# Performance work log

Measured on AMD Instinct MI355X. Metric: run time of the kernel, lower is better.

## Reference

```python
import jax, jax.numpy as jnp
import numpy as np

B, T, C = 2, 2048, 1024
H = 16
D = C // H  # head_dim = 64
EPS = 1e-06
MAX_SEQ = 2048


def make_rotary(dim, max_seq_len, base=10000):
    inv_freq = 1.0 / (base ** (jnp.arange(0, dim, 2, dtype=jnp.float32) / dim))
    pos = jnp.arange(max_seq_len, dtype=jnp.float32)
    sinusoid = jnp.einsum('i,j->ij', pos, inv_freq)  # (S, dim//2)
    return jnp.sin(sinusoid), jnp.cos(sinusoid)


def apply_rotary(x, sin, cos):
    # x: (B, T, H, D); sin/cos: (MAX_SEQ, D//2)
    t = x.shape[1]
    s = sin[:t][:, None, :]  # (T,1,D//2) broadcasts over B and H
    c = cos[:t][:, None, :]
    d = x.shape[-1]
    x1, x2 = x[..., :d // 2], x[..., d // 2:]
    return jnp.concatenate([x1 * c - x2 * s, x2 * c + x1 * s], axis=-1)


def yat_dense(x, kernel, bias, alpha, eps=EPS):
    # Yat layer: squared dot product over squared euclidean distance.
    dot = x @ kernel                                   # (..., out)
    x_sq = jnp.sum(x * x, axis=-1, keepdims=True)      # (..., 1)
    k_sq = jnp.sum(kernel * kernel, axis=0)            # (out,)
    dist = x_sq + k_sq - 2.0 * dot
    y = (dot * dot) / (dist + eps)
    out_f = kernel.shape[1]
    scale = (jnp.sqrt(jnp.float32(out_f)) / jnp.log(1.0 + jnp.float32(out_f))) ** alpha
    return y * scale + bias


def setup_inputs() -> dict:
    key = jax.random.key(0)
    ks = jax.random.split(key, 7)
    x = jax.random.normal(ks[0], (B, T, C), dtype=jnp.float32)
    mask = jnp.tril(jnp.ones((T, T), dtype=bool))[None].repeat(B, axis=0)  # (B,T,T) causal
    s = 1.0 / np.sqrt(C)
    w_attn = jax.random.normal(ks[1], (C, 3 * C), dtype=jnp.float32) * s
    b_attn = jnp.zeros((3 * C,), dtype=jnp.float32)
    a_attn = jnp.ones((1,), dtype=jnp.float32)
    w_proj = jax.random.normal(ks[2], (C, C), dtype=jnp.float32) * s
    b_proj = jnp.zeros((C,), dtype=jnp.float32)
    a_proj = jnp.ones((1,), dtype=jnp.float32)
    return {"x": x, "mask": mask, "w_attn": w_attn, "b_attn": b_attn,
            "a_attn": a_attn, "w_proj": w_proj, "b_proj": b_proj, "a_proj": a_proj}


def reference(x, mask, w_attn, b_attn, a_attn, w_proj, b_proj, a_proj):
    b, t, c = x.shape
    sin, cos = make_rotary(D, MAX_SEQ)
    qkv = yat_dense(x, w_attn, b_attn, a_attn)          # (B,T,3C)
    qkv = qkv.reshape(b, t, 3, H, D)
    q, k, v = jnp.moveaxis(qkv, 2, 0)                   # each (B,T,H,D)
    q = apply_rotary(q, sin, cos)
    k = apply_rotary(k, sin, cos)
    # heads-major layout for attention
    q = q.transpose(0, 2, 1, 3)                          # (B,H,T,D)
    k = k.transpose(0, 2, 1, 3)
    v = v.transpose(0, 2, 1, 3)
    scale = jnp.sqrt(jnp.float32(D))
    attn = jnp.einsum('bhqd,bhkd->bhqk', q, k) / scale   # (B,H,T,T)
    m = mask[:, None, :, :]                              # (B,1,T,T)
    attn = jnp.where(m, attn, jnp.finfo(jnp.float32).min)
    attn = jax.nn.softmax(attn, axis=-1)
    # dropout is identity in deterministic/eval mode
    out = jnp.einsum('bhqk,bhkd->bhqd', attn, v)         # (B,H,T,D)
    out = out.transpose(0, 2, 1, 3).reshape(b, t, c)     # (B,T,C)
    out = yat_dense(out, w_proj, b_proj, a_proj)
    return out
```

## Files before the change

kernel.cpp:

```cpp
#include <hip/hip_runtime.h>
#include <math.h>

#define TSEQ  2048
#define BATCH 2
#define NH    16
#define HD    64
#define CDIM  1024
#define N3C   3072
#define EPSY  1e-6f

typedef unsigned short u16;
typedef unsigned int u32;
typedef __attribute__((ext_vector_type(8))) short bf16x8;
typedef __attribute__((ext_vector_type(4))) float f32x4;

#define MFMA16(a, b, c) __builtin_amdgcn_mfma_f32_16x16x32_bf16(a, b, c, 0, 0, 0)

__device__ __forceinline__ u16 f2bf(float f) {
    unsigned u = __float_as_uint(f);
    return (u16)((u + 0x7fffu + ((u >> 16) & 1u)) >> 16);
}
__device__ __forceinline__ float bf2f(u16 h) {
    return __uint_as_float(((unsigned)h) << 16);
}
__device__ __forceinline__ void gload16(const void* g, void* l) {
    __builtin_amdgcn_global_load_lds(
        (const __attribute__((address_space(1))) unsigned int*)g,
        (__attribute__((address_space(3))) unsigned int*)l, 16, 0, 0);
}

__global__ __launch_bounds__(256) void prep_kernel(
    const float* __restrict__ x, const float* __restrict__ wa,
    const float* __restrict__ wp, u16* __restrict__ Ahi,
    u16* __restrict__ Wthi, u16* __restrict__ Wphi,
    float* __restrict__ ksq, float* __restrict__ xsq,
    float* __restrict__ osq, float2* __restrict__ ropeSC) {
    __shared__ float smem[64 * 68];
    int bid = blockIdx.x, tid = threadIdx.x;

    if (bid < 4096) {
        int lane = tid & 63, wv = tid >> 6;
        size_t base = (size_t)bid * CDIM + tid * 4;
        float4 v = *(const float4*)(x + base);
        ushort4 hi;
        hi.x = f2bf(v.x); hi.y = f2bf(v.y); hi.z = f2bf(v.z); hi.w = f2bf(v.w);
        *(ushort4*)(Ahi + base) = hi;
        float s = v.x * v.x + v.y * v.y + v.z * v.z + v.w * v.w;
        #pragma unroll
        for (int off = 32; off; off >>= 1) s += __shfl_down(s, off, 64);
        if (lane == 0) smem[wv] = s;
        __syncthreads();
        if (tid == 0) xsq[bid] = smem[0] + smem[1] + smem[2] + smem[3];
    } else if (bid < 5120) {
        const float* W; u16* Whi; int K, N, bx, by;
        if (bid < 4864) {
            int t = bid - 4096; W = wa; Whi = Wthi; K = CDIM; N = N3C;
            bx = t % 48; by = t / 48;
        } else {
            int t = bid - 4864; W = wp; Whi = Wphi; K = CDIM; N = CDIM;
            bx = t % 16; by = t / 16;
        }
        int k0 = by * 64, n0 = bx * 64;
        int r = tid >> 4, c4 = (tid & 15) * 4;
        #pragma unroll
        for (int i = 0; i < 4; ++i) {
            int k = k0 + r + i * 16;
            float4 v = *(const float4*)(W + (size_t)k * N + n0 + c4);
            *(float4*)&smem[(r + i * 16) * 68 + c4] = v;
        }
        __syncthreads();
        int n = tid >> 4, k4 = (tid & 15) * 4;
        #pragma unroll
        for (int i = 0; i < 4; ++i) {
            int nn = n + i * 16;
            ushort4 hi;
            hi.x = f2bf(smem[(k4 + 0) * 68 + nn]);
            hi.y = f2bf(smem[(k4 + 1) * 68 + nn]);
            hi.z = f2bf(smem[(k4 + 2) * 68 + nn]);
            hi.w = f2bf(smem[(k4 + 3) * 68 + nn]);
            *(ushort4*)(Whi + (size_t)(n0 + nn) * K + k0 + k4) = hi;
        }
    } else if (bid < 5184) {
        int b2 = bid - 5120;
        int c = tid & 63, kq = tid >> 6;
        const float* W; int N, col, outoff;
        if (b2 < 48) { W = wa; N = N3C;  col = b2 * 64 + c;        outoff = 0;   }
        else         { W = wp; N = CDIM; col = (b2 - 48) * 64 + c; outoff = N3C; }
        float s = 0.f;
        int i0 = kq * 256;
        #pragma unroll 4
        for (int i = i0; i < i0 + 256; ++i) {
            float v = W[(size_t)i * N + col];
            s = fmaf(v, v, s);
        }
        smem[tid] = s;
        __syncthreads();
        if (kq == 0)
            ksq[outoff + col] = smem[c] + smem[64 + c] + smem[128 + c] + smem[192 + c];
    } else {
        int idx = (bid - 5184) * 256 + tid;
        if (idx < BATCH * TSEQ) osq[idx] = 0.f;
        int t = idx >> 5, j = idx & 31;
        float inv = exp2f(-(float)j * 0.4152410118609203f);
        float ang = (float)t * inv;
        ropeSC[idx] = make_float2(cosf(ang), sinf(ang));
    }
}

__global__ __launch_bounds__(256, 4) void gemm1_fused(
    const u16* __restrict__ Ah, const u16* __restrict__ Bh,
    const float* __restrict__ bias, const float* __restrict__ rowsq,
    const float* __restrict__ colsq, const float* __restrict__ alphap,
    const float2* __restrict__ ropeSC,
    u16* __restrict__ Qb, u16* __restrict__ Kb, u16* __restrict__ Vt) {
    constexpr int BK = 32;
    const int K = CDIM;
    __shared__ u16 Ash[128 * BK], Bsh[128 * BK];
    int tid = threadIdx.x;
    int lane = tid & 63, wv = tid >> 6;
    int quad = lane >> 4, l15 = lane & 15;
    int wr = wv >> 1, wc = wv & 1;
    int bm = blockIdx.y * 128, bn = blockIdx.x * 128;
    int rsub = lane >> 2;
    int lc8 = (lane & 3) * 8;
    int gc8 = (((lane & 3) - (rsub >> 1)) & 3) * 8;
    int pf8 = ((quad + (l15 >> 1)) & 3) * 8;

    f32x4 acc[4][4];
    #pragma unroll
    for (int i = 0; i < 4; ++i)
        #pragma unroll
        for (int j = 0; j < 4; ++j) acc[i][j] = (f32x4){0.f, 0.f, 0.f, 0.f};

    for (int kt = 0; kt < K; kt += BK) {
        #pragma unroll
        for (int i = 0; i < 2; ++i) {
            int r = i * 64 + wv * 16 + rsub;
            gload16(Ah + (size_t)(bm + r) * K + kt + gc8, &Ash[r * BK + lc8]);
            gload16(Bh + (size_t)(bn + r) * K + kt + gc8, &Bsh[r * BK + lc8]);
        }
        __syncthreads();
        bf16x8 fah[4], fbh[4];
        #pragma unroll
        for (int i = 0; i < 4; ++i)
            fah[i] = *(const bf16x8*)&Ash[(wr * 64 + i * 16 + l15) * BK + pf8];
        #pragma unroll
        for (int j = 0; j < 4; ++j)
            fbh[j] = *(const bf16x8*)&Bsh[(wc * 64 + j * 16 + l15) * BK + pf8];
        #pragma unroll
        for (int i = 0; i < 4; ++i)
            #pragma unroll
            for (int j = 0; j < 4; ++j)
                acc[i][j] = MFMA16(fah[i], fbh[j], acc[i][j]);
        __syncthreads();
    }

    float alpha = alphap[0];
    float scale = powf(sqrtf((float)N3C) / logf(1.0f + (float)N3C), alpha);
    int segc0 = bn + wc * 64;
    int seg = segc0 >> 10;
    int h = (segc0 >> 6) & 15;
    int bglob = bm >> 11;
    int bh = bglob * NH + h;

    if (seg < 2) {
        u16* dst = (seg == 0) ? Qb : Kb;
        float qs = (seg == 0) ? 0.125f : 1.0f;
        #pragma unroll
        for (int i = 0; i < 4; ++i) {
            int tb = bm + wr * 64 + i * 16 + quad * 4;
            #pragma unroll
            for (int r = 0; r < 4; ++r) {
                int row = tb + r;
                int t = row & (TSEQ - 1);
                float rs = rowsq[row];
                float y[4];
                #pragma unroll
                for (int j = 0; j < 4; ++j) {
                    int col = segc0 + j * 16 + l15;
                    float dot = acc[i][j][r];
                    float dist = rs + colsq[col] - 2.0f * dot + EPSY;
                    y[j] = dot * dot / dist * scale + bias[col];
                }
                float2 sc0 = ropeSC[t * 32 + l15];
                float2 sc1 = ropeSC[t * 32 + 16 + l15];
                float c0 = sc0.x, s0 = sc0.y, c1 = sc1.x, s1 = sc1.y;
                size_t ob = ((size_t)bh * TSEQ + t) * HD;
                dst[ob + l15]      = f2bf((y[0] * c0 - y[2] * s0) * qs);
                dst[ob + 16 + l15] = f2bf((y[1] * c1 - y[3] * s1) * qs);
                dst[ob + 32 + l15] = f2bf((y[2] * c0 + y[0] * s0) * qs);
                dst[ob + 48 + l15] = f2bf((y[3] * c1 + y[1] * s1) * qs);
            }
        }
    } else {
        #pragma unroll
        for (int i = 0; i < 4; ++i) {
            int tb = bm + wr * 64 + i * 16 + quad * 4;
            int t0 = tb & (TSEQ - 1);
            #pragma unroll
            for (int j = 0; j < 4; ++j) {
                int col = segc0 + j * 16 + l15;
                int d = j * 16 + l15;
                float cs = colsq[col], bi = bias[col];
                ushort4 pk;
                u16* pp = (u16*)&pk;
                #pragma unroll
                for (int r = 0; r < 4; ++r) {
                    float dot = acc[i][j][r];
                    float dist = rowsq[tb + r] + cs - 2.0f * dot + EPSY;
                    pp[r] = f2bf(dot * dot / dist * scale + bi);
                }
                *(ushort4*)(Vt + ((size_t)bh * HD + d) * TSEQ + t0) = pk;
            }
        }
    }
}

__global__ __launch_bounds__(256, 4) void gemm_yat_mfma(
    const u16* __restrict__ Ah, const u16* __restrict__ Bh,
    const float* __restrict__ bias, const float* __restrict__ rowsq,
    const float* __restrict__ colsq, const float* __restrict__ alphap,
    float* __restrict__ outp, int M, int N, int K, float outf) {
    constexpr int BM = 128, BN = 64, BK = 32;
    __shared__ u16 Ash[BM * BK], Bsh[BN * BK];
    int tid = threadIdx.x;
    int lane = tid & 63, wv = tid >> 6;
    int quad = lane >> 4, l15 = lane & 15;
    int bm = blockIdx.y * BM, bn = blockIdx.x * BN;
    int rsub = lane >> 2;
    int lc8 = (lane & 3) * 8;
    int gc8 = (((lane & 3) - (rsub >> 1)) & 3) * 8;
    int pf8 = ((quad + (l15 >> 1)) & 3) * 8;

    f32x4 acc[2][4];
    #pragma unroll
    for (int i = 0; i < 2; ++i)
        #pragma unroll
        for (int j = 0; j < 4; ++j) acc[i][j] = (f32x4){0.f, 0.f, 0.f, 0.f};

    for (int kt = 0; kt < K; kt += BK) {
        #pragma unroll
        for (int i = 0; i < 2; ++i) {
            int r = i * 64 + wv * 16 + rsub;
            gload16(Ah + (size_t)(bm + r) * K + kt + gc8, &Ash[r * BK + lc8]);
        }
        {
            int r = wv * 16 + rsub;
            gload16(Bh + (size_t)(bn + r) * K + kt + gc8, &Bsh[r * BK + lc8]);
        }
        __syncthreads();
        bf16x8 fah[2], fbh[4];
        #pragma unroll
        for (int i = 0; i < 2; ++i)
            fah[i] = *(const bf16x8*)&Ash[(wv * 32 + i * 16 + l15) * BK + pf8];
        #pragma unroll
        for (int j = 0; j < 4; ++j)
            fbh[j] = *(const bf16x8*)&Bsh[(j * 16 + l15) * BK + pf8];
        #pragma unroll
        for (int i = 0; i < 2; ++i)
            #pragma unroll
            for (int j = 0; j < 4; ++j)
                acc[i][j] = MFMA16(fah[i], fbh[j], acc[i][j]);
        __syncthreads();
    }

    float alpha = alphap[0];
    float scale = powf(sqrtf(outf) / logf(1.0f + outf), alpha);
    #pragma unroll
    for (int j = 0; j < 4; ++j) {
        int col = bn + j * 16 + l15;
        float cs = colsq[col], bi = bias[col];
        #pragma unroll
        for (int i = 0; i < 2; ++i) {
            #pragma unroll
            for (int r = 0; r < 4; ++r) {
                int row = bm + wv * 32 + i * 16 + quad * 4 + r;
                float dot = acc[i][j][r];
                float dist = rowsq[row] + cs - 2.0f * dot + EPSY;
                outp[(size_t)row * N + col] = dot * dot / dist * scale + bi;
            }
        }
    }
}

__global__ __launch_bounds__(128) void attn_mfma(
    const u16* __restrict__ Qb, const u16* __restrict__ Kb,
    const u16* __restrict__ Vt, u16* __restrict__ Chi,
    float* __restrict__ osq) {
    __shared__ u16 Ksh[64 * 64];
    __shared__ u16 Vsh[64 * 64];
    int tid = threadIdx.x;
    int lane = tid & 63, wv = tid >> 6;
    int quad = lane >> 4, l15 = lane & 15;
    int bh = blockIdx.x;
    int b = bh >> 4, h = bh & 15;
    const u16* Qh = Qb + (size_t)bh * TSEQ * HD;
    const u16* Kh = Kb + (size_t)bh * TSEQ * HD;
    const u16* Vh = Vt + (size_t)bh * HD * TSEQ;
    const f32x4 zf = {0.f, 0.f, 0.f, 0.f};

    int qb = 31 - (blockIdx.y >> 1);
    int half = blockIdx.y & 1;
    int qw = qb * 64 + half * 32 + wv * 16;
    bf16x8 bq0 = *(const bf16x8*)(Qh + (size_t)(qw + l15) * HD + quad * 8);
    bf16x8 bq1 = *(const bf16x8*)(Qh + (size_t)(qw + l15) * HD + 32 + quad * 8);

    f32x4 o[4] = {zf, zf, zf, zf};
    float l = 0.f;

    for (int kt = 0; kt <= qb; ++kt) {
        int k0 = kt * 64;
        __syncthreads();
        #pragma unroll
        for (int p = 0; p < 4; ++p) {
            int lin = p * 128 + tid;
            int rowi = lin >> 3, ch = lin & 7;
            int gk = (ch + rowi) & 7;
            gload16(Kh + (size_t)(k0 + rowi) * HD + gk * 8, &Ksh[lin * 8]);
            gload16(Vh + (size_t)rowi * TSEQ + k0 + gk * 8, &Vsh[lin * 8]);
        }
        __syncthreads();

        f32x4 st[4];
        #pragma unroll
        for (int mt = 0; mt < 4; ++mt) {
            int key = mt * 16 + l15;
            bf16x8 a0 = *(const bf16x8*)&Ksh[key * 64 + ((quad - key) & 7) * 8];
            bf16x8 a1 = *(const bf16x8*)&Ksh[key * 64 + ((4 + quad - key) & 7) * 8];
            st[mt] = MFMA16(a0, bq0, zf);
            st[mt] = MFMA16(a1, bq1, st[mt]);
        }
        if (kt == qb) {
            int q = qw + l15;
            #pragma unroll
            for (int mt = 0; mt < 4; ++mt)
                #pragma unroll
                for (int r = 0; r < 4; ++r)
                    if (k0 + mt * 16 + quad * 4 + r > q) st[mt][r] = -1e30f;
        }
        u32 pp[4][2];
        #pragma unroll
        for (int mt = 0; mt < 4; ++mt) {
            float p0 = __expf(st[mt][0]);
            float p1 = __expf(st[mt][1]);
            float p2 = __expf(st[mt][2]);
            float p3 = __expf(st[mt][3]);
            l += (p0 + p1) + (p2 + p3);
            pp[mt][0] = (u32)f2bf(p0) | ((u32)f2bf(p1) << 16);
            pp[mt][1] = (u32)f2bf(p2) | ((u32)f2bf(p3) << 16);
        }
        #pragma unroll
        for (int s = 0; s < 2; ++s) {
            u32 bw[4];
            #pragma unroll
            for (int w = 0; w < 4; ++w) {
                int srcl = (((quad & 1) * 2 + (w >> 1)) << 4) + l15;
                u32 vlo = (u32)__shfl((int)pp[2 * s][w & 1], srcl, 64);
                u32 vhi = (u32)__shfl((int)pp[2 * s + 1][w & 1], srcl, 64);
                bw[w] = (quad & 2) ? vhi : vlo;
            }
            bf16x8 bfr;
            *(u32*)&((short*)&bfr)[0] = bw[0];
            *(u32*)&((short*)&bfr)[2] = bw[1];
            *(u32*)&((short*)&bfr)[4] = bw[2];
            *(u32*)&((short*)&bfr)[6] = bw[3];
            #pragma unroll
            for (int dt = 0; dt < 4; ++dt) {
                int d = dt * 16 + l15;
                bf16x8 av = *(const bf16x8*)&Vsh[d * 64 + ((s * 4 + quad - d) & 7) * 8];
                o[dt] = MFMA16(av, bfr, o[dt]);
            }
        }
    }

    l += __shfl_xor(l, 16, 64);
    l += __shfl_xor(l, 32, 64);
    float inv = 1.0f / l;
    int row = (b << 11) + qw + l15;
    float ss = 0.f;
    #pragma unroll
    for (int dt = 0; dt < 4; ++dt) {
        float v0 = o[dt][0] * inv, v1 = o[dt][1] * inv;
        float v2 = o[dt][2] * inv, v3 = o[dt][3] * inv;
        ss += v0 * v0 + v1 * v1 + v2 * v2 + v3 * v3;
        ushort4 pk;
        pk.x = f2bf(v0); pk.y = f2bf(v1); pk.z = f2bf(v2); pk.w = f2bf(v3);
        *(ushort4*)(Chi + (size_t)row * CDIM + h * HD + dt * 16 + quad * 4) = pk;
    }
    ss += __shfl_xor(ss, 16, 64);
    ss += __shfl_xor(ss, 32, 64);
    if (quad == 0) atomicAdd(osq + row, ss);
}

extern "C" void kernel_launch(void* const* d_in, const int* in_sizes, int n_in,
                              void* d_out, int out_size, void* d_ws, size_t ws_size,
                              hipStream_t stream) {
    const float* x      = (const float*)d_in[0];
    const float* w_attn = (const float*)d_in[2];
    const float* b_attn = (const float*)d_in[3];
    const float* a_attn = (const float*)d_in[4];
    const float* w_proj = (const float*)d_in[5];
    const float* b_proj = (const float*)d_in[6];
    const float* a_proj = (const float*)d_in[7];
    float* outp = (float*)d_out;

    char* ws = (char*)d_ws;
    float* ksq = (float*)(ws);
    float* xsq = (float*)(ws + 16384);
    float* osq = (float*)(ws + 32768);
    char* pA  = ws + 65536;
    u16* Ahi = (u16*)pA;
    u16* Chi = (u16*)pA;
    char* pWt = pA + 16777216;
    u16* Wthi = (u16*)pWt;
    char* pWp = pWt + 6291456;
    u16* Wphi = (u16*)pWp;
    char* pQ = pWp + 2097152;
    u16* Qb = (u16*)pQ;
    u16* Kb = (u16*)(pQ + 8388608);
    u16* Vt = (u16*)(pQ + 16777216);
    float2* ropeSC = (float2*)(pQ + 25165824);

    prep_kernel<<<5440, 256, 0, stream>>>(
        x, w_attn, w_proj, Ahi, Wthi, Wphi, ksq, xsq, osq, ropeSC);
    gemm1_fused<<<dim3(N3C / 128, (BATCH * TSEQ) / 128), 256, 0, stream>>>(
        Ahi, Wthi, b_attn, xsq, ksq, a_attn, ropeSC, Qb, Kb, Vt);
    attn_mfma<<<dim3(BATCH * NH, 64), 128, 0, stream>>>(Qb, Kb, Vt, Chi, osq);
    gemm_yat_mfma<<<dim3(CDIM / 64, (BATCH * TSEQ) / 128), 256, 0, stream>>>(
        Chi, Wphi, b_proj, osq, ksq + N3C, a_proj, outp,
        BATCH * TSEQ, CDIM, CDIM, (float)CDIM);
}
```

Baseline: 238.7 us.

## Double-buffer K/V tiles in attention and use packed bf16 conversion

The attention kernel now keeps two LDS buffers for K and V. It issues the asynchronous global-to-LDS loads for the next key tile before computing on the current one, so a single barrier per iteration replaces the two it had before. The scalar round-to-nearest bf16 packing is replaced by the v_cvt_pk_bf16_f32 instruction, and the MFMA sections are wrapped in s_setprio to raise wave priority. In exchange, LDS use per block doubles, which may reduce occupancy, and correctness relies on the barrier waiting for the outstanding LDS-DMA loads.

```diff
diff --git a/kernel.cpp b/kernel.cpp
--- a/kernel.cpp
+++ b/kernel.cpp
@@ -22,6 +22,11 @@
 }
 __device__ __forceinline__ float bf2f(u16 h) {
     return __uint_as_float(((unsigned)h) << 16);
+}
+__device__ __forceinline__ u32 cvtpk_bf16(float lo, float hi) {
+    u32 r;
+    asm("v_cvt_pk_bf16_f32 %0, %1, %2" : "=v"(r) : "v"(lo), "v"(hi));
+    return r;
 }
 __device__ __forceinline__ void gload16(const void* g, void* l) {
     __builtin_amdgcn_global_load_lds(
@@ -287,8 +292,8 @@
     const u16* __restrict__ Qb, const u16* __restrict__ Kb,
     const u16* __restrict__ Vt, u16* __restrict__ Chi,
     float* __restrict__ osq) {
-    __shared__ u16 Ksh[64 * 64];
-    __shared__ u16 Vsh[64 * 64];
+    __shared__ u16 Ksh[2][64 * 64];
+    __shared__ u16 Vsh[2][64 * 64];
     int tid = threadIdx.x;
     int lane = tid & 63, wv = tid >> 6;
     int quad = lane >> 4, l15 = lane & 15;
@@ -308,28 +313,41 @@
     f32x4 o[4] = {zf, zf, zf, zf};
     float l = 0.f;
 
+    int lin0 = tid;
+
+    auto STAGE = [&](int buf, int kt) {
+        int k0s = kt * 64;
+        #pragma unroll
+        for (int p = 0; p < 4; ++p) {
+            int lin = p * 128 + lin0;
+            int rowi = lin >> 3, ch = lin & 7;
+            int gk = (ch + rowi) & 7;
+            gload16(Kh + (size_t)(k0s + rowi) * HD + gk * 8, &Ksh[buf][lin * 8]);
+            gload16(Vh + (size_t)rowi * TSEQ + k0s + gk * 8, &Vsh[buf][lin * 8]);
+        }
+    };
+
+    STAGE(0, 0);
+    __syncthreads();
+    int cur = 0;
+
     for (int kt = 0; kt <= qb; ++kt) {
         int k0 = kt * 64;
-        __syncthreads();
-        #pragma unroll
-        for (int p = 0; p < 4; ++p) {
-            int lin = p * 128 + tid;
-            int rowi = lin >> 3, ch = lin & 7;
-            int gk = (ch + rowi) & 7;
-            gload16(Kh + (size_t)(k0 + rowi) * HD + gk * 8, &Ksh[lin * 8]);
-            gload16(Vh + (size_t)rowi * TSEQ + k0 + gk * 8, &Vsh[lin * 8]);
-        }
-        __syncthreads();
+        if (kt < qb) STAGE(cur ^ 1, kt + 1);
+        const u16* Kc = Ksh[cur];
+        const u16* Vc = Vsh[cur];
 
         f32x4 st[4];
+        __builtin_amdgcn_s_setprio(1);
         #pragma unroll
         for (int mt = 0; mt < 4; ++mt) {
             int key = mt * 16 + l15;
-            bf16x8 a0 = *(const bf16x8*)&Ksh[key * 64 + ((quad - key) & 7) * 8];
-            bf16x8 a1 = *(const bf16x8*)&Ksh[key * 64 + ((4 + quad - key) & 7) * 8];
+            bf16x8 a0 = *(const bf16x8*)&Kc[key * 64 + ((quad - key) & 7) * 8];
+            bf16x8 a1 = *(const bf16x8*)&Kc[key * 64 + ((4 + quad - key) & 7) * 8];
             st[mt] = MFMA16(a0, bq0, zf);
             st[mt] = MFMA16(a1, bq1, st[mt]);
         }
+        __builtin_amdgcn_s_setprio(0);
         if (kt == qb) {
             int q = qw + l15;
             #pragma unroll
@@ -346,8 +364,8 @@
             float p2 = __expf(st[mt][2]);
             float p3 = __expf(st[mt][3]);
             l += (p0 + p1) + (p2 + p3);
-            pp[mt][0] = (u32)f2bf(p0) | ((u32)f2bf(p1) << 16);
-            pp[mt][1] = (u32)f2bf(p2) | ((u32)f2bf(p3) << 16);
+            pp[mt][0] = cvtpk_bf16(p0, p1);
+            pp[mt][1] = cvtpk_bf16(p2, p3);
         }
         #pragma unroll
         for (int s = 0; s < 2; ++s) {
@@ -364,13 +382,17 @@
             *(u32*)&((short*)&bfr)[2] = bw[1];
             *(u32*)&((short*)&bfr)[4] = bw[2];
             *(u32*)&((short*)&bfr)[6] = bw[3];
+            __builtin_amdgcn_s_setprio(1);
             #pragma unroll
             for (int dt = 0; dt < 4; ++dt) {
                 int d = dt * 16 + l15;
-                bf16x8 av = *(const bf16x8*)&Vsh[d * 64 + ((s * 4 + quad - d) & 7) * 8];
+                bf16x8 av = *(const bf16x8*)&Vc[d * 64 + ((s * 4 + quad - d) & 7) * 8];
                 o[dt] = MFMA16(av, bfr, o[dt]);
             }
-        }
+            __builtin_amdgcn_s_setprio(0);
+        }
+        __syncthreads();
+        cur ^= 1;
     }
 
     l += __shfl_xor(l, 16, 64);
@@ -383,9 +405,10 @@
         float v0 = o[dt][0] * inv, v1 = o[dt][1] * inv;
         float v2 = o[dt][2] * inv, v3 = o[dt][3] * inv;
         ss += v0 * v0 + v1 * v1 + v2 * v2 + v3 * v3;
-        ushort4 pk;
-        pk.x = f2bf(v0); pk.y = f2bf(v1); pk.z = f2bf(v2); pk.w = f2bf(v3);
-        *(ushort4*)(Chi + (size_t)row * CDIM + h * HD + dt * 16 + quad * 4) = pk;
+        uint2 pk2;
+        pk2.x = cvtpk_bf16(v0, v1);
+        pk2.y = cvtpk_bf16(v2, v3);
+        *(uint2*)(Chi + (size_t)row * CDIM + h * HD + dt * 16 + quad * 4) = pk2;
     }
     ss += __shfl_xor(ss, 16, 64);
     ss += __shfl_xor(ss, 32, 64);
```

Measured after the change: 233.7 us. 1.02x faster.
